# Kernel tuning notes

Measured on AMD Instinct MI355X. Metric: run time of the kernel, lower is better.

Reference implementation:

```python
import jax, jax.numpy as jnp
import numpy as np

N, E, D, H, G, C = 100000, 1200000, 64, 64, 128, 10


def setup_inputs() -> dict:
    key = jax.random.key(0)
    ks = jax.random.split(key, 20)
    def lin(k, fin, fout):
        kw, kb = jax.random.split(k)
        s = 1.0 / np.sqrt(fin)
        return (jax.random.uniform(kw, (fin, fout), jnp.float32, -s, s),
                jax.random.uniform(kb, (fout,), jnp.float32, -s, s))
    w1a, b1a = lin(ks[0], D, H)
    w1b, b1b = lin(ks[1], H, H)
    w2a, b2a = lin(ks[2], H, H)
    w2b, b2b = lin(ks[3], H, H)
    w3a, b3a = lin(ks[4], H, H)
    w3b, b3b = lin(ks[5], H, H)
    wc, bc = lin(ks[6], H, C)
    x = jax.random.normal(ks[7], (N, D), jnp.float32)
    edge_index = jax.random.randint(ks[8], (2, E), 0, N, dtype=jnp.int32)
    batch = jnp.sort(jax.random.randint(ks[9], (N,), 0, G, dtype=jnp.int32))
    return {"x": x, "w1a": w1a, "b1a": b1a, "w1b": w1b, "b1b": b1b,
            "w2a": w2a, "b2a": b2a, "w2b": w2b, "b2b": b2b,
            "w3a": w3a, "b3a": b3a, "w3b": w3b, "b3b": b3b,
            "wc": wc, "bc": bc, "edge_index": edge_index, "batch": batch}


def _gin_layer(x, src, dst, wa, ba, wb, bb):
    # GINConv (eps=0): mlp(x + sum_{j in N(i)} x_j), then outer ReLU from GIN.forward
    agg = jax.ops.segment_sum(x[src], dst, num_segments=N)  # [N, d]
    h = x + agg
    h = jax.nn.relu(h @ wa + ba) @ wb + bb
    return jax.nn.relu(h)


def reference(x, w1a, b1a, w1b, b1b, w2a, b2a, w2b, b2b,
              w3a, b3a, w3b, b3b, wc, bc, edge_index, batch):
    src, dst = edge_index[0], edge_index[1]
    x = _gin_layer(x, src, dst, w1a, b1a, w1b, b1b)
    x = _gin_layer(x, src, dst, w2a, b2a, w2b, b2b)
    x = _gin_layer(x, src, dst, w3a, b3a, w3b, b3b)
    # global mean pool over graphs
    sums = jax.ops.segment_sum(x, batch, num_segments=G)              # [G, H]
    cnts = jax.ops.segment_sum(jnp.ones((N,), x.dtype), batch, num_segments=G)
    pooled = sums / jnp.maximum(cnts, 1.0)[:, None]
    return pooled @ wc + bc  # [G, C]
```

## Files before the change

kernel.cpp:

```cpp
#include <hip/hip_runtime.h>
#include <hip/hip_bf16.h>


#define N_NODES 100000
#define N_EDGES 1200000
#define N_GRAPH 128
#define N_CLS   10
#define NBUCK   391
#define BCAP    4096
#define BSH     12
#define NTILES  6250
#define TOBF_BLKS 1563
#define BINA_BLKS 586

typedef __bf16 bf16_t;
typedef __bf16 bf16x8 __attribute__((ext_vector_type(8)));
typedef float  f32x4  __attribute__((ext_vector_type(4)));

__global__ void prep_kernel(const float* __restrict__ x, bf16_t* __restrict__ xb,
                            int* __restrict__ bcnt, float* __restrict__ gsum,
                            const float* __restrict__ w1a, const float* __restrict__ w1b,
                            const float* __restrict__ w2a, const float* __restrict__ w2b,
                            const float* __restrict__ w3a, const float* __restrict__ w3b,
                            bf16_t* __restrict__ wfragG,
                            bf16_t* __restrict__ hPad, bf16_t* __restrict__ xAPad,
                            const int* __restrict__ ei, int* __restrict__ bpair) {
    __shared__ int lcnt[NBUCK];
    __shared__ int lbase[NBUCK];
    const int tid = threadIdx.x;
    const int blk = blockIdx.x;

    if (blk >= TOBF_BLKS) {
        for (int b = tid; b < NBUCK; b += 512) lcnt[b] = 0;
        __syncthreads();
        const int e0 = ((blk - TOBF_BLKS) * 512 + tid) * 4;
        int4 s4, d4; int b[4], r[4];
        const bool valid = e0 < N_EDGES;
        if (valid) {
            s4 = *(const int4*)(ei + e0);
            d4 = *(const int4*)(ei + N_EDGES + e0);
            b[0] = d4.x >> 8; b[1] = d4.y >> 8; b[2] = d4.z >> 8; b[3] = d4.w >> 8;
            r[0] = atomicAdd(&lcnt[b[0]], 1);
            r[1] = atomicAdd(&lcnt[b[1]], 1);
            r[2] = atomicAdd(&lcnt[b[2]], 1);
            r[3] = atomicAdd(&lcnt[b[3]], 1);
        }
        __syncthreads();
        for (int bb = tid; bb < NBUCK; bb += 512) {
            const int c = lcnt[bb];
            lbase[bb] = c ? atomicAdd(&bcnt[bb], c) : 0;
        }
        __syncthreads();
        if (valid) {
            const int ss[4] = {s4.x, s4.y, s4.z, s4.w};
            const int dd[4] = {d4.x, d4.y, d4.z, d4.w};
#pragma unroll
            for (int j = 0; j < 4; ++j) {
                const int slot = lbase[b[j]] + r[j];
                if (slot < BCAP)
                    bpair[(b[j] << BSH) + slot] = (ss[j] << 8) | (dd[j] & 255);
            }
        }
        return;
    }

    if (blk == 0) {
        f32x4* g4 = (f32x4*)gsum;
        for (int i = tid; i < N_GRAPH * 16; i += 512)
            g4[i] = (f32x4){0.f, 0.f, 0.f, 0.f};
        if (tid < 64) {
            xb[N_NODES * 64 + tid]    = (bf16_t)0.f;
            hPad[N_NODES * 64 + tid]  = (bf16_t)0.f;
            xAPad[N_NODES * 64 + tid] = (bf16_t)0.f;
        }
    } else if (blk <= 3 && tid < 256) {
        const int L = blk - 1;
        const float* wA = L == 0 ? w1a : (L == 1 ? w2a : w3a);
        const float* wB = L == 0 ? w1b : (L == 1 ? w2b : w3b);
        const int k  = tid >> 2;
        const int n0 = (tid & 3) << 4;
        const int ks = k >> 5, qd = (k >> 3) & 3, jj = k & 7;
        const int fi = ((n0 >> 4) << 1) + ks;
#pragma unroll
        for (int m = 0; m < 2; ++m) {
            const float* w = m ? wB : wA;
            const f32x4 v0 = *(const f32x4*)(w + k * 64 + n0);
            const f32x4 v1 = *(const f32x4*)(w + k * 64 + n0 + 4);
            const f32x4 v2 = *(const f32x4*)(w + k * 64 + n0 + 8);
            const f32x4 v3 = *(const f32x4*)(w + k * 64 + n0 + 12);
            bf16_t* dst = wfragG + ((L * 2 + m) * 8 + fi) * 512 + jj;
#pragma unroll
            for (int l = 0; l < 4; ++l) {
                dst[(qd * 16 + l) * 8]      = (bf16_t)v0[l];
                dst[(qd * 16 + 4 + l) * 8]  = (bf16_t)v1[l];
                dst[(qd * 16 + 8 + l) * 8]  = (bf16_t)v2[l];
                dst[(qd * 16 + 12 + l) * 8] = (bf16_t)v3[l];
            }
        }
    }

    const int i = (blk * 512 + tid) * 8;
    if (i < N_NODES * 64) {
        const f32x4 a = *(const f32x4*)(x + i);
        const f32x4 b = *(const f32x4*)(x + i + 4);
        bf16x8 o;
#pragma unroll
        for (int j = 0; j < 4; ++j) { o[j] = (bf16_t)a[j]; o[4 + j] = (bf16_t)b[j]; }
        *(bf16x8*)(xb + i) = o;
    }
}

__global__ void sortfill_kernel(const int* __restrict__ bpair,
                                const int* __restrict__ bcnt,
                                int* __restrict__ offset, int* __restrict__ csr) {
    __shared__ int red[1024];
    __shared__ int hist[256];
    __shared__ int l[256];
    __shared__ int cursor[256];
    const int b = blockIdx.x;
    const int t = threadIdx.x;
    const int base = b << BSH;

    int part = 0;
    for (int i = t; i < b; i += 1024) {
        int c = bcnt[i];
        part += (c < BCAP ? c : BCAP);
    }
    red[t] = part;
    __syncthreads();
    for (int d = 512; d > 0; d >>= 1) {
        if (t < d) red[t] += red[t + d];
        __syncthreads();
    }
    const int cbase = red[0];
    int cnt = bcnt[b];
    cnt = cnt < BCAP ? cnt : BCAP;
    if (b == NBUCK - 1 && t == 0) offset[N_NODES] = cbase + cnt;
    __syncthreads();

    if (t < 256) hist[t] = 0;
    __syncthreads();
    for (int i = t; i < cnt; i += 1024)
        atomicAdd(&hist[bpair[base + i] & 255], 1);
    __syncthreads();

    int v = 0;
    if (t < 256) { v = hist[t]; l[t] = v; }
    __syncthreads();
    for (int d = 1; d < 256; d <<= 1) {
        int u = 0;
        if (t < 256) { u = l[t]; if (t >= d) u += l[t - d]; }
        __syncthreads();
        if (t < 256) l[t] = u;
        __syncthreads();
    }
    if (t < 256) {
        const int gpos = cbase + l[t] - v;
        const int node = (b << 8) + t;
        if (node < N_NODES) offset[node] = gpos;
        cursor[t] = gpos;
    }
    __syncthreads();

    for (int i = t; i < cnt; i += 1024) {
        const int p = bpair[base + i];
        const int pos = atomicAdd(&cursor[p & 255], 1);
        csr[pos] = p >> 8;
    }
}

#define G8(S, J, ACC)                                                          \
    {                                                                          \
        const int t0 = __shfl(S, (J) + 0), t1 = __shfl(S, (J) + 1);            \
        const int t2 = __shfl(S, (J) + 2), t3 = __shfl(S, (J) + 3);            \
        const int t4 = __shfl(S, (J) + 4), t5 = __shfl(S, (J) + 5);            \
        const int t6 = __shfl(S, (J) + 6), t7 = __shfl(S, (J) + 7);            \
        const float u0 = (float)x[t0 * 64 + f], u1 = (float)x[t1 * 64 + f];    \
        const float u2 = (float)x[t2 * 64 + f], u3 = (float)x[t3 * 64 + f];    \
        const float u4 = (float)x[t4 * 64 + f], u5 = (float)x[t5 * 64 + f];    \
        const float u6 = (float)x[t6 * 64 + f], u7 = (float)x[t7 * 64 + f];    \
        ACC += ((u0 + u1) + (u2 + u3)) + ((u4 + u5) + (u6 + u7));              \
    }

#define ROWPAIR(I, SA, CA, DA, OA, SB, CB, DB, OB)                             \
    {                                                                          \
        float accA = (float)x[(r0w + I) * 64 + f];                             \
        float accB = (float)x[(r0w + I + 4) * 64 + f];                         \
        const int cmax = (CA) > (CB) ? (CA) : (CB);                            \
        for (int j = 0; j < cmax; j += 8) {                                    \
            if (j < (CA)) { G8(SA, j, accA) }                                  \
            if (j < (CB)) { G8(SB, j, accB) }                                  \
        }                                                                      \
        if ((DA) > 64 || (DB) > 64) {                      \
            for (int base = 64; base < (DA) || base < (DB); base += 64) {      \
                const int ra = (DA) - base, rb2 = (DB) - base;                 \
                const int ca2 = ra <= 0 ? 0 : (ra < 64 ? ra : 64);             \
                const int cb2 = rb2 <= 0 ? 0 : (rb2 < 64 ? rb2 : 64);          \
                int sA2 = N_NODES, sB2 = N_NODES;                              \
                if (f < ca2) sA2 = csr[(OA) + base + f];                       \
                if (f < cb2) sB2 = csr[(OB) + base + f];                       \
                const int cm2 = ca2 > cb2 ? ca2 : cb2;                         \
                for (int j = 0; j < cm2; j += 8) {                             \
                    if (j < ca2) { G8(sA2, j, accA) }                          \
                    if (j < cb2) { G8(sB2, j, accB) }                          \
                }                                                              \
            }                                                                  \
        }                                                                      \
        hsw[half][I][lane]     = (bf16_t)accA;                                 \
        hsw[half][I + 4][lane] = (bf16_t)accB;                                 \
    }

template <int POOL>
__global__ void gmlp_kernel(const bf16_t* __restrict__ x,
                            const int* __restrict__ offset,
                            const int* __restrict__ csr,
                            const bf16_t* __restrict__ wf,
                            const float* __restrict__ ba, const float* __restrict__ bb,
                            bf16_t* __restrict__ xout,
                            const int* __restrict__ batch,
                            float* __restrict__ gsum) {
    __shared__ __align__(16) bf16_t hsw[2][16][72];
    __shared__ __align__(16) bf16_t h2w[2][16][72];

    const int tid  = threadIdx.x;
    const int half = tid >> 6;
    const int lane = tid & 63;
    const int l15  = lane & 15;
    const int quad = lane >> 4;

    const int r0w = blockIdx.x * 16 + half * 8;
    const int f   = lane;

    int offv = 0;
    if (lane < 9) offv = offset[r0w + lane];
    const int o0 = __shfl(offv, 0), o1 = __shfl(offv, 1), o2 = __shfl(offv, 2);
    const int o3 = __shfl(offv, 3), o4 = __shfl(offv, 4), o5 = __shfl(offv, 5);
    const int o6 = __shfl(offv, 6), o7 = __shfl(offv, 7), o8 = __shfl(offv, 8);
    const int d0 = o1 - o0, d1 = o2 - o1, d2 = o3 - o2, d3 = o4 - o3;
    const int d4 = o5 - o4, d5 = o6 - o5, d6 = o7 - o6, d7 = o8 - o7;
    const int c0 = d0 < 64 ? d0 : 64, c1 = d1 < 64 ? d1 : 64;
    const int c2 = d2 < 64 ? d2 : 64, c3 = d3 < 64 ? d3 : 64;
    const int c4 = d4 < 64 ? d4 : 64, c5 = d5 < 64 ? d5 : 64;
    const int c6 = d6 < 64 ? d6 : 64, c7 = d7 < 64 ? d7 : 64;

    int s0 = N_NODES, s1 = N_NODES, s2 = N_NODES, s3 = N_NODES;
    int s4 = N_NODES, s5 = N_NODES, s6 = N_NODES, s7 = N_NODES;
    if (f < c0) s0 = csr[o0 + f];
    if (f < c1) s1 = csr[o1 + f];
    if (f < c2) s2 = csr[o2 + f];
    if (f < c3) s3 = csr[o3 + f];
    if (f < c4) s4 = csr[o4 + f];
    if (f < c5) s5 = csr[o5 + f];
    if (f < c6) s6 = csr[o6 + f];
    if (f < c7) s7 = csr[o7 + f];

    ROWPAIR(0, s0, c0, d0, o0, s4, c4, d4, o4)
    ROWPAIR(1, s1, c1, d1, o1, s5, c5, d5, o5)
    ROWPAIR(2, s2, c2, d2, o2, s6, c6, d6, o6)
    ROWPAIR(3, s3, c3, d3, o3, s7, c7, d7, o7)

    {
        bf16x8 af[2];
#pragma unroll
        for (int ks = 0; ks < 2; ++ks)
            af[ks] = *(const bf16x8*)(&hsw[half][l15][ks * 32 + quad * 8]);
#pragma unroll
        for (int ct = 0; ct < 4; ++ct) {
            const bf16x8 b0 = *(const bf16x8*)(wf + (0 * 8 + ct * 2 + 0) * 512 + lane * 8);
            const bf16x8 b1 = *(const bf16x8*)(wf + (0 * 8 + ct * 2 + 1) * 512 + lane * 8);
            f32x4 acc = {0.f, 0.f, 0.f, 0.f};
            acc = __builtin_amdgcn_mfma_f32_16x16x32_bf16(af[0], b0, acc, 0, 0, 0);
            acc = __builtin_amdgcn_mfma_f32_16x16x32_bf16(af[1], b1, acc, 0, 0, 0);
            const float bv = ba[ct * 16 + l15];
#pragma unroll
            for (int r = 0; r < 4; ++r) {
                float h = acc[r] + bv;
                h = h > 0.f ? h : 0.f;
                h2w[half][quad * 4 + r][ct * 16 + l15] = (bf16_t)h;
            }
        }
    }

    {
        bf16x8 a2[2];
#pragma unroll
        for (int ks = 0; ks < 2; ++ks)
            a2[ks] = *(const bf16x8*)(&h2w[half][l15][ks * 32 + quad * 8]);
#pragma unroll
        for (int ct = 0; ct < 4; ++ct) {
            const bf16x8 b0 = *(const bf16x8*)(wf + (1 * 8 + ct * 2 + 0) * 512 + lane * 8);
            const bf16x8 b1 = *(const bf16x8*)(wf + (1 * 8 + ct * 2 + 1) * 512 + lane * 8);
            f32x4 acc = {0.f, 0.f, 0.f, 0.f};
            acc = __builtin_amdgcn_mfma_f32_16x16x32_bf16(a2[0], b0, acc, 0, 0, 0);
            acc = __builtin_amdgcn_mfma_f32_16x16x32_bf16(a2[1], b1, acc, 0, 0, 0);
            const float bv = bb[ct * 16 + l15];
#pragma unroll
            for (int r = 0; r < 4; ++r) {
                float h = acc[r] + bv;
                h = h > 0.f ? h : 0.f;
                hsw[half][quad * 4 + r][ct * 16 + l15] = (bf16_t)h;
            }
        }
    }

    if (POOL) {
        int cur = -1;
        float acc = 0.f;
        for (int r = 0; r < 8; ++r) {
            const int row = r0w + r;
            const int g = batch[row];
            const float v = (float)hsw[half][r][lane];
            if (g != cur) {
                if (cur >= 0) unsafeAtomicAdd(gsum + cur * 64 + lane, acc);
                acc = 0.f;
                cur = g;
            }
            acc += v;
        }
        if (cur >= 0) unsafeAtomicAdd(gsum + cur * 64 + lane, acc);
    } else {
        const int row8 = lane >> 3;
        const int colg = (lane & 7) * 8;
        const bf16x8 v = *(const bf16x8*)&hsw[half][row8][colg];
        *(bf16x8*)(xout + (r0w + row8) * 64 + colg) = v;
    }
}

__global__ void cls_kernel(const float* __restrict__ gsum,
                           const int* __restrict__ batch,
                           const float* __restrict__ wc, const float* __restrict__ bc,
                           float* __restrict__ out) {
    const int g = blockIdx.x;
    const int c = threadIdx.x;
    if (c >= N_CLS) return;
    int lo = 0, hi = N_NODES;
    while (lo < hi) { const int m = (lo + hi) >> 1; if (batch[m] < g) lo = m + 1; else hi = m; }
    const int lb = lo;
    lo = 0; hi = N_NODES;
    while (lo < hi) { const int m = (lo + hi) >> 1; if (batch[m] <= g) lo = m + 1; else hi = m; }
    const int cnt = lo - lb;
    const float inv = 1.f / (float)(cnt > 1 ? cnt : 1);
    float acc = bc[c];
    for (int k = 0; k < 64; ++k)
        acc += gsum[g * 64 + k] * inv * wc[k * N_CLS + c];
    out[g * N_CLS + c] = acc;
}

extern "C" void kernel_launch(void* const* d_in, const int* in_sizes, int n_in,
                              void* d_out, int out_size, void* d_ws, size_t ws_size,
                              hipStream_t stream) {
    const float* x   = (const float*)d_in[0];
    const float* w1a = (const float*)d_in[1];
    const float* b1a = (const float*)d_in[2];
    const float* w1b = (const float*)d_in[3];
    const float* b1b = (const float*)d_in[4];
    const float* w2a = (const float*)d_in[5];
    const float* b2a = (const float*)d_in[6];
    const float* w2b = (const float*)d_in[7];
    const float* b2b = (const float*)d_in[8];
    const float* w3a = (const float*)d_in[9];
    const float* b3a = (const float*)d_in[10];
    const float* w3b = (const float*)d_in[11];
    const float* b3b = (const float*)d_in[12];
    const float* wc  = (const float*)d_in[13];
    const float* bc  = (const float*)d_in[14];
    const int*   ei    = (const int*)d_in[15];
    const int*   batch = (const int*)d_in[16];
    float* out = (float*)d_out;

    char*   ws     = (char*)d_ws;
    int*    bcnt   = (int*)ws;
    int*    offset = (int*)(ws + 3136);
    int*    csr    = (int*)(ws + 403152);
    int*    bpair  = (int*)(ws + 5203152);
    bf16_t* xbf    = (bf16_t*)(ws + 11609296);
    bf16_t* h      = (bf16_t*)(ws + 24409424);
    bf16_t* xA     = (bf16_t*)(ws + 37209552);
    float*  gsum   = (float*)(ws + 50009680);
    bf16_t* wfragG = (bf16_t*)(ws + 50042448);

    hipMemsetAsync(bcnt, 0, NBUCK * sizeof(int), stream);

    prep_kernel<<<TOBF_BLKS + BINA_BLKS, 512, 0, stream>>>(
        x, xbf, bcnt, gsum, w1a, w1b, w2a, w2b, w3a, w3b, wfragG, h, xA, ei, bpair);

    sortfill_kernel<<<NBUCK, 1024, 0, stream>>>(bpair, bcnt, offset, csr);

    gmlp_kernel<0><<<NTILES, 128, 0, stream>>>(xbf, offset, csr, wfragG,         b1a, b1b, xA, nullptr, nullptr);
    gmlp_kernel<0><<<NTILES, 128, 0, stream>>>(xA,  offset, csr, wfragG + 8192,  b2a, b2b, h,  nullptr, nullptr);
    gmlp_kernel<1><<<NTILES, 128, 0, stream>>>(h,   offset, csr, wfragG + 16384, b3a, b3b, nullptr, batch, gsum);

    cls_kernel<<<N_GRAPH, 64, 0, stream>>>(gsum, batch, wc, bc, out);
}
```

Baseline: 269.4 us.

## Share 16-row MFMA tile across both waves and use nontemporal CSR loads/stores

```diff
diff --git a/kernel.cpp b/kernel.cpp
--- a/kernel.cpp
+++ b/kernel.cpp
@@ -197,8 +197,8 @@
                 const int ca2 = ra <= 0 ? 0 : (ra < 64 ? ra : 64);             \
                 const int cb2 = rb2 <= 0 ? 0 : (rb2 < 64 ? rb2 : 64);          \
                 int sA2 = N_NODES, sB2 = N_NODES;                              \
-                if (f < ca2) sA2 = csr[(OA) + base + f];                       \
-                if (f < cb2) sB2 = csr[(OB) + base + f];                       \
+                if (f < ca2) sA2 = __builtin_nontemporal_load(csr + (OA) + base + f); \
+                if (f < cb2) sB2 = __builtin_nontemporal_load(csr + (OB) + base + f); \
                 const int cm2 = ca2 > cb2 ? ca2 : cb2;                         \
                 for (int j = 0; j < cm2; j += 8) {                             \
                     if (j < ca2) { G8(sA2, j, accA) }                          \
@@ -206,8 +206,8 @@
                 }                                                              \
             }                                                                  \
         }                                                                      \
-        hsw[half][I][lane]     = (bf16_t)accA;                                 \
-        hsw[half][I + 4][lane] = (bf16_t)accB;                                 \
+        hs[half * 8 + I][lane]     = (bf16_t)accA;                             \
+        hs[half * 8 + I + 4][lane] = (bf16_t)accB;                             \
     }
 
 template <int POOL>
@@ -219,8 +219,8 @@
                             bf16_t* __restrict__ xout,
                             const int* __restrict__ batch,
                             float* __restrict__ gsum) {
-    __shared__ __align__(16) bf16_t hsw[2][16][72];
-    __shared__ __align__(16) bf16_t h2w[2][16][72];
+    __shared__ __align__(16) bf16_t hs[16][72];
+    __shared__ __align__(16) bf16_t h2[16][72];
 
     const int tid  = threadIdx.x;
     const int half = tid >> 6;
@@ -228,7 +228,8 @@
     const int l15  = lane & 15;
     const int quad = lane >> 4;
 
-    const int r0w = blockIdx.x * 16 + half * 8;
+    const int rb  = blockIdx.x * 16;
+    const int r0w = rb + half * 8;
     const int f   = lane;
 
     int offv = 0;
@@ -245,27 +246,30 @@
 
     int s0 = N_NODES, s1 = N_NODES, s2 = N_NODES, s3 = N_NODES;
     int s4 = N_NODES, s5 = N_NODES, s6 = N_NODES, s7 = N_NODES;
-    if (f < c0) s0 = csr[o0 + f];
-    if (f < c1) s1 = csr[o1 + f];
-    if (f < c2) s2 = csr[o2 + f];
-    if (f < c3) s3 = csr[o3 + f];
-    if (f < c4) s4 = csr[o4 + f];
-    if (f < c5) s5 = csr[o5 + f];
-    if (f < c6) s6 = csr[o6 + f];
-    if (f < c7) s7 = csr[o7 + f];
+    if (f < c0) s0 = __builtin_nontemporal_load(csr + o0 + f);
+    if (f < c1) s1 = __builtin_nontemporal_load(csr + o1 + f);
+    if (f < c2) s2 = __builtin_nontemporal_load(csr + o2 + f);
+    if (f < c3) s3 = __builtin_nontemporal_load(csr + o3 + f);
+    if (f < c4) s4 = __builtin_nontemporal_load(csr + o4 + f);
+    if (f < c5) s5 = __builtin_nontemporal_load(csr + o5 + f);
+    if (f < c6) s6 = __builtin_nontemporal_load(csr + o6 + f);
+    if (f < c7) s7 = __builtin_nontemporal_load(csr + o7 + f);
 
     ROWPAIR(0, s0, c0, d0, o0, s4, c4, d4, o4)
     ROWPAIR(1, s1, c1, d1, o1, s5, c5, d5, o5)
     ROWPAIR(2, s2, c2, d2, o2, s6, c6, d6, o6)
     ROWPAIR(3, s3, c3, d3, o3, s7, c7, d7, o7)
 
+    __syncthreads();
+
     {
         bf16x8 af[2];
 #pragma unroll
         for (int ks = 0; ks < 2; ++ks)
-            af[ks] = *(const bf16x8*)(&hsw[half][l15][ks * 32 + quad * 8]);
-#pragma unroll
-        for (int ct = 0; ct < 4; ++ct) {
+            af[ks] = *(const bf16x8*)(&hs[l15][ks * 32 + quad * 8]);
+#pragma unroll
+        for (int c = 0; c < 2; ++c) {
+            const int ct = half * 2 + c;
             const bf16x8 b0 = *(const bf16x8*)(wf + (0 * 8 + ct * 2 + 0) * 512 + lane * 8);
             const bf16x8 b1 = *(const bf16x8*)(wf + (0 * 8 + ct * 2 + 1) * 512 + lane * 8);
             f32x4 acc = {0.f, 0.f, 0.f, 0.f};
@@ -276,18 +280,21 @@
             for (int r = 0; r < 4; ++r) {
                 float h = acc[r] + bv;
                 h = h > 0.f ? h : 0.f;
-                h2w[half][quad * 4 + r][ct * 16 + l15] = (bf16_t)h;
+                h2[quad * 4 + r][ct * 16 + l15] = (bf16_t)h;
             }
         }
     }
+
+    __syncthreads();
 
     {
         bf16x8 a2[2];
 #pragma unroll
         for (int ks = 0; ks < 2; ++ks)
-            a2[ks] = *(const bf16x8*)(&h2w[half][l15][ks * 32 + quad * 8]);
-#pragma unroll
-        for (int ct = 0; ct < 4; ++ct) {
+            a2[ks] = *(const bf16x8*)(&h2[l15][ks * 32 + quad * 8]);
+#pragma unroll
+        for (int c = 0; c < 2; ++c) {
+            const int ct = half * 2 + c;
             const bf16x8 b0 = *(const bf16x8*)(wf + (1 * 8 + ct * 2 + 0) * 512 + lane * 8);
             const bf16x8 b1 = *(const bf16x8*)(wf + (1 * 8 + ct * 2 + 1) * 512 + lane * 8);
             f32x4 acc = {0.f, 0.f, 0.f, 0.f};
@@ -298,10 +305,12 @@
             for (int r = 0; r < 4; ++r) {
                 float h = acc[r] + bv;
                 h = h > 0.f ? h : 0.f;
-                hsw[half][quad * 4 + r][ct * 16 + l15] = (bf16_t)h;
+                hs[quad * 4 + r][ct * 16 + l15] = (bf16_t)h;
             }
         }
     }
+
+    __syncthreads();
 
     if (POOL) {
         int cur = -1;
@@ -309,7 +318,7 @@
         for (int r = 0; r < 8; ++r) {
             const int row = r0w + r;
             const int g = batch[row];
-            const float v = (float)hsw[half][r][lane];
+            const float v = (float)hs[half * 8 + r][lane];
             if (g != cur) {
                 if (cur >= 0) unsafeAtomicAdd(gsum + cur * 64 + lane, acc);
                 acc = 0.f;
@@ -319,10 +328,10 @@
         }
         if (cur >= 0) unsafeAtomicAdd(gsum + cur * 64 + lane, acc);
     } else {
-        const int row8 = lane >> 3;
-        const int colg = (lane & 7) * 8;
-        const bf16x8 v = *(const bf16x8*)&hsw[half][row8][colg];
-        *(bf16x8*)(xout + (r0w + row8) * 64 + colg) = v;
+        const int row16 = half * 8 + (lane >> 3);
+        const int colg  = (lane & 7) * 8;
+        const bf16x8 v = *(const bf16x8*)&hs[row16][colg];
+        __builtin_nontemporal_store(v, (bf16x8*)(xout + (rb + row16) * 64 + colg));
     }
 }
 
```

New measurement: 268.1 us. No clear change (-0.5%).
